# Performance work log

Measured on AMD Instinct MI355X. Metric: run time of the kernel, lower is better.

The kernel has to match this reference:

```python
import jax, jax.numpy as jnp
import numpy as np

EMBED_DIM = 512
HEADS = 8
ATTN_DIM = EMBED_DIM // HEADS
PF_DIM = 2048
B, L = 4, 2048
LN_EPS = 1e-5


def _linear(x, W, b):
    # nn.Linear: x @ W.T + b, W is [out, in]
    return jnp.einsum('bld,od->blo', x, W) + b


def _layer_norm(x, g, b):
    mu = jnp.mean(x, axis=-1, keepdims=True)
    var = jnp.mean(jnp.square(x - mu), axis=-1, keepdims=True)
    return (x - mu) * jax.lax.rsqrt(var + LN_EPS) * g + b


def _qkv(src, Wq, bq, Wk, bk, Wv, bv):
    def split(t):
        Bb, Ll, _ = t.shape
        return t.reshape(Bb, Ll, HEADS, ATTN_DIM).transpose(0, 2, 1, 3)  # [B,H,L,Dh]
    return (split(_linear(src, Wq, bq)),
            split(_linear(src, Wk, bk)),
            split(_linear(src, Wv, bv)))


def _attention(inp, Q, K1, K2, V1, V2, Wo, bo, ln_g, ln_b, W1, b1, W2, b2):
    # non-softmax linear attention: (Q K1^T) V1 + (Q K2^T) V2
    attn = (jnp.einsum('bhqk,bhkd->bhqd', jnp.einsum('bhqd,bhkd->bhqk', Q, K1), V1)
            + jnp.einsum('bhqk,bhkd->bhqd', jnp.einsum('bhqd,bhkd->bhqk', Q, K2), V2))
    Bb = Q.shape[0]
    attn = attn.transpose(0, 2, 1, 3).reshape(Bb, -1, HEADS * ATTN_DIM)  # [B,L,D]
    x = _linear(attn, Wo, bo)
    x = _layer_norm(inp + x, ln_g, ln_b)          # dropout p=0 (eval)
    ff = _linear(jax.nn.relu(_linear(x, W1, b1)), W2, b2)
    x = _layer_norm(x + ff, ln_g, ln_b)
    return x


def setup_inputs() -> dict:
    key = jax.random.key(0)
    ks = jax.random.split(key, 16)
    s = 0.02
    return {
        'question': jax.random.normal(ks[0], (B, L, EMBED_DIM), jnp.float32),
        'query': jax.random.normal(ks[1], (B, L, EMBED_DIM), jnp.float32),
        'Wq': jax.random.normal(ks[2], (EMBED_DIM, EMBED_DIM), jnp.float32) * s,
        'bq': jnp.zeros((EMBED_DIM,), jnp.float32),
        'Wk': jax.random.normal(ks[3], (EMBED_DIM, EMBED_DIM), jnp.float32) * s,
        'bk': jnp.zeros((EMBED_DIM,), jnp.float32),
        'Wv': jax.random.normal(ks[4], (EMBED_DIM, EMBED_DIM), jnp.float32) * s,
        'bv': jnp.zeros((EMBED_DIM,), jnp.float32),
        'Wo': jax.random.normal(ks[5], (EMBED_DIM, EMBED_DIM), jnp.float32) * s,
        'bo': jnp.zeros((EMBED_DIM,), jnp.float32),
        'ln_g': jnp.ones((EMBED_DIM,), jnp.float32),
        'ln_b': jnp.zeros((EMBED_DIM,), jnp.float32),
        'W1': jax.random.normal(ks[6], (PF_DIM, EMBED_DIM), jnp.float32) * s,
        'b1': jnp.zeros((PF_DIM,), jnp.float32),
        'W2': jax.random.normal(ks[7], (EMBED_DIM, PF_DIM), jnp.float32) * s,
        'b2': jnp.zeros((EMBED_DIM,), jnp.float32),
    }


def reference(question, query, Wq, bq, Wk, bk, Wv, bv, Wo, bo, ln_g, ln_b, W1, b1, W2, b2):
    Q1, K1, V1 = _qkv(question, Wq, bq, Wk, bk, Wv, bv)
    Q2, K2, V2 = _qkv(query, Wq, bq, Wk, bk, Wv, bv)
    question_attn = _attention(question, Q1, K1, K2, V1, V2, Wo, bo, ln_g, ln_b, W1, b1, W2, b2)
    query_attn = _attention(query, Q2, K2, K1, V2, V1, Wo, bo, ln_g, ln_b, W1, b1, W2, b2)
    return jnp.concatenate([question_attn, query_attn], axis=-1)
```

## Files before the change

kernel.cpp:

```cpp
#include <hip/hip_runtime.h>
#include <stdint.h>


#define Bq 4
#define Lq 2048
#define Dq 512
#define PFq 2048
#define Mrows 16384
#define MiBu 1048576ull
#define NSLICE 16

typedef __attribute__((ext_vector_type(8))) short frag_ab;
typedef __attribute__((ext_vector_type(4))) float frag_cd;
typedef __attribute__((ext_vector_type(8))) unsigned short ushort8v;

__device__ __forceinline__ unsigned short f2b(float f) {
    union { float f; uint32_t u; } x; x.f = f;
    uint32_t r = x.u + 0x7fffu + ((x.u >> 16) & 1u);
    return (unsigned short)(r >> 16);
}
__device__ __forceinline__ float b2f(unsigned short u) {
    union { uint32_t u; float f; } x; x.u = ((uint32_t)u) << 16;
    return x.f;
}

#define GLD16(g, l)                                                              \
    __builtin_amdgcn_global_load_lds(                                            \
        (const __attribute__((address_space(1))) void*)(const void*)(g),         \
        (__attribute__((address_space(3))) void*)(void*)(l), 16, 0, 0)

#define STG(BUFOFS, REGOFS, GB, ROWOFS, TILE, KS)                                \
    { GLD16((GB) + (size_t)(ROWOFS) * (KS) + (size_t)(TILE) * 64,                \
            Sh + (BUFOFS) + (REGOFS) + ld);                                      \
      GLD16((GB) + ((size_t)(ROWOFS) + 64) * (KS) + (size_t)(TILE) * 64,         \
            Sh + (BUFOFS) + (REGOFS) + ld + 4096); }

#define VMW(N) asm volatile("s_waitcnt vmcnt(" #N ")" ::: "memory")

#define PHASE(CB, M0, LOADB, STAGE_STMT, WAIT_STMT)                              \
    {                                                                            \
        frag_ab a00 = *(const frag_ab*)&Sh[(CB) + (wm + (M0)*16 + lr) * 64 + xo0];      \
        frag_ab a01 = *(const frag_ab*)&Sh[(CB) + (wm + (M0)*16 + lr) * 64 + xo1];      \
        frag_ab a10 = *(const frag_ab*)&Sh[(CB) + (wm + (M0)*16 + 16 + lr) * 64 + xo0]; \
        frag_ab a11 = *(const frag_ab*)&Sh[(CB) + (wm + (M0)*16 + 16 + lr) * 64 + xo1]; \
        if (LOADB) {                                                             \
            _Pragma("unroll")                                                    \
            for (int j = 0; j < 4; ++j) {                                        \
                bf[j][0] = *(const frag_ab*)&Sh[(CB) + 16384 + (wn + j*16 + lr)*64 + xo0]; \
                bf[j][1] = *(const frag_ab*)&Sh[(CB) + 16384 + (wn + j*16 + lr)*64 + xo1]; \
            }                                                                    \
        }                                                                        \
        STAGE_STMT;                                                              \
        WAIT_STMT;                                                               \
        __builtin_amdgcn_sched_barrier(0);                                       \
        __builtin_amdgcn_s_barrier();                                            \
        asm volatile("s_waitcnt lgkmcnt(0)" ::: "memory");                       \
        __builtin_amdgcn_sched_barrier(0);                                       \
        __builtin_amdgcn_s_setprio(1);                                           \
        _Pragma("unroll")                                                        \
        for (int j = 0; j < 4; ++j) {                                            \
            acc[(M0)][j]   = __builtin_amdgcn_mfma_f32_16x16x32_bf16(a00, bf[j][0], acc[(M0)][j], 0,0,0);   \
            acc[(M0)][j]   = __builtin_amdgcn_mfma_f32_16x16x32_bf16(a01, bf[j][1], acc[(M0)][j], 0,0,0);   \
            acc[(M0)+1][j] = __builtin_amdgcn_mfma_f32_16x16x32_bf16(a10, bf[j][0], acc[(M0)+1][j], 0,0,0); \
            acc[(M0)+1][j] = __builtin_amdgcn_mfma_f32_16x16x32_bf16(a11, bf[j][1], acc[(M0)+1][j], 0,0,0); \
        }                                                                        \
        __builtin_amdgcn_s_setprio(0);                                           \
        __builtin_amdgcn_sched_barrier(0);                                       \
        __builtin_amdgcn_s_barrier();                                            \
        __builtin_amdgcn_sched_barrier(0);                                       \
    }

__global__ __launch_bounds__(512, 2) void gemm_256(
    const unsigned short* __restrict__ A, const unsigned short* __restrict__ Wt,
    const float* __restrict__ bias, unsigned short* __restrict__ outB,
    int M, int N, int relu)
{
    __shared__ __align__(16) unsigned short Sh[65536];
    const int tid = threadIdx.x;
    const int lane = tid & 63;
    const int w = tid >> 6;
    const int wm = (w >> 2) * 128;
    const int wn = (w & 3) * 64;
    const int lr = lane & 15;
    const int quad = lane >> 4;
    const int xo0 = ((quad ^ (lr & 7)) << 3);
    const int xo1 = (((4 | quad) ^ (lr & 7)) << 3);

    const int b0 = blockIdx.x;
    const int xcd = b0 & 7, slot = b0 >> 3;
    const int mloc = (M >> 8) >> 3;
    const size_t bm = (size_t)(xcd * mloc + slot % mloc) * 256;
    const size_t bn = (size_t)(slot / mloc) * 256;

    const int ar = tid >> 3;
    const int sw = ((tid & 7) ^ (ar & 7)) << 3;
    const unsigned short* Ag = A  + (bm + ar) * (size_t)512 + sw;
    const unsigned short* Bg = Wt + (bn + ar) * (size_t)512 + sw;
    const int ld = tid * 8;

    frag_cd acc[8][4] = {};
    frag_ab bf[4][2];

    STG(0,     16384, Bg, 0,   0, 512);
    STG(0,     24576, Bg, 128, 0, 512);
    STG(0,     0,     Ag, 0,   0, 512);
    STG(0,     8192,  Ag, 128, 0, 512);
    STG(32768, 16384, Bg, 0,   1, 512);
    STG(32768, 24576, Bg, 128, 1, 512);
    VMW(4);
    __builtin_amdgcn_sched_barrier(0);
    __builtin_amdgcn_s_barrier();
    __builtin_amdgcn_sched_barrier(0);

    for (int I = 0; I < 3; ++I) {
        const int tb = 2 * I + 1, tc = 2 * I + 2, td = 2 * I + 3;
        PHASE(0,     0, 1, STG(32768, 0,     Ag, 0,   tb, 512), (void)0);
        PHASE(0,     2, 0, STG(32768, 8192,  Ag, 128, tb, 512), (void)0);
        PHASE(0,     4, 0, STG(0,     16384, Bg, 0,   tc, 512), (void)0);
        PHASE(0,     6, 0, STG(0,     24576, Bg, 128, tc, 512), VMW(4));
        PHASE(32768, 0, 1, STG(0,     0,     Ag, 0,   tc, 512), (void)0);
        PHASE(32768, 2, 0, STG(0,     8192,  Ag, 128, tc, 512), (void)0);
        PHASE(32768, 4, 0, STG(32768, 16384, Bg, 0,   td, 512), (void)0);
        PHASE(32768, 6, 0, STG(32768, 24576, Bg, 128, td, 512), VMW(4));
    }
    PHASE(0,     0, 1, STG(32768, 0,    Ag, 0,   7, 512), (void)0);
    PHASE(0,     2, 0, STG(32768, 8192, Ag, 128, 7, 512), (void)0);
    PHASE(0,     4, 0, (void)0, (void)0);
    PHASE(0,     6, 0, (void)0, VMW(0));
    PHASE(32768, 0, 1, (void)0, (void)0);
    PHASE(32768, 2, 0, (void)0, (void)0);
    PHASE(32768, 4, 0, (void)0, (void)0);
    PHASE(32768, 6, 0, (void)0, (void)0);

    float bv[4];
#pragma unroll
    for (int j = 0; j < 4; ++j) bv[j] = bias[(int)bn + wn + j * 16 + lr];
    unsigned short* Cs = Sh + w * 8192;
#pragma unroll
    for (int m = 0; m < 8; ++m)
#pragma unroll
        for (int j = 0; j < 4; ++j)
#pragma unroll
            for (int r = 0; r < 4; ++r) {
                float v = acc[m][j][r] + bv[j];
                if (relu) v = fmaxf(v, 0.f);
                Cs[(m * 16 + quad * 4 + r) * 64 + j * 16 + lr] = f2b(v);
            }
    const int rl = lane >> 3, c8 = (lane & 7) * 8;
#pragma unroll
    for (int k = 0; k < 16; ++k) {
        const int row = rl + k * 8;
        ushort8v val = *(const ushort8v*)&Cs[row * 64 + c8];
        *(ushort8v*)(outB + (size_t)(bm + wm + row) * N + bn + wn + c8) = val;
    }
}

__global__ __launch_bounds__(512, 2) void gemm_n128(
    const unsigned short* __restrict__ A, const unsigned short* __restrict__ Wt,
    const float* __restrict__ bias,
    const float* __restrict__ resA, const float* __restrict__ resB,
    const unsigned short* __restrict__ res16,
    unsigned short* __restrict__ outB, int N, int K, int mode, int perb)
{
    __shared__ __align__(16) unsigned short Sh[49152];
    const int tid = threadIdx.x;
    const int lane = tid & 63;
    const int w = tid >> 6;
    const int wm = (w >> 1) * 64;
    const int wn = (w & 1) * 64;
    const int lr = lane & 15;
    const int quad = lane >> 4;
    const int xo0 = ((quad ^ (lr & 7)) << 3);
    const int xo1 = (((4 | quad) ^ (lr & 7)) << 3);

    const int b0 = blockIdx.x;
    const int xcd = b0 & 7, slot = b0 >> 3;
    const size_t bm = (size_t)(xcd * 8 + (slot & 7)) * 256;
    const size_t bn = (size_t)(slot >> 3) * 128;

    if (perb) {
        const int bsel = ((int)(bm >> 11)) & 3;
        Wt += (size_t)bsel << 18;
        bias += bsel << 9;
    }

    const int ar = tid >> 3;
    const int sw = ((tid & 7) ^ (ar & 7)) << 3;
    const unsigned short* Ag = A  + (bm + ar) * (size_t)K + sw;
    const unsigned short* Bg = Wt + (bn + ar) * (size_t)K + sw;
    const int ld = tid * 8;

    frag_cd acc[4][4] = {};
    frag_ab bf[4][2];

    STG(0,     16384, Bg, 0,   0, K);
    STG(0,     0,     Ag, 0,   0, K);
    STG(0,     8192,  Ag, 128, 0, K);
    STG(24576, 16384, Bg, 0,   1, K);
    VMW(2);
    __builtin_amdgcn_sched_barrier(0);
    __builtin_amdgcn_s_barrier();
    __builtin_amdgcn_sched_barrier(0);

    const int nIter = K >> 7;
    for (int I = 0; I < nIter - 1; ++I) {
        const int tb = 2 * I + 1, tc = 2 * I + 2, td = 2 * I + 3;
        PHASE(0,     0, 1, { STG(24576, 0, Ag, 0, tb, K); STG(24576, 8192, Ag, 128, tb, K); }, (void)0);
        PHASE(0,     2, 0, STG(0, 16384, Bg, 0, tc, K), VMW(2));
        PHASE(24576, 0, 1, { STG(0, 0, Ag, 0, tc, K); STG(0, 8192, Ag, 128, tc, K); }, (void)0);
        PHASE(24576, 2, 0, STG(24576, 16384, Bg, 0, td, K), VMW(2));
    }
    {
        const int tb = (K >> 6) - 1;
        PHASE(0,     0, 1, { STG(24576, 0, Ag, 0, tb, K); STG(24576, 8192, Ag, 128, tb, K); }, (void)0);
        PHASE(0,     2, 0, (void)0, VMW(0));
        PHASE(24576, 0, 1, (void)0, (void)0);
        PHASE(24576, 2, 0, (void)0, (void)0);
    }

    float bv[4];
#pragma unroll
    for (int j = 0; j < 4; ++j) bv[j] = bias[(int)bn + wn + j * 16 + lr];
    unsigned short* Cs = Sh + w * 4096;
#pragma unroll
    for (int m = 0; m < 4; ++m)
#pragma unroll
        for (int j = 0; j < 4; ++j)
#pragma unroll
            for (int r = 0; r < 4; ++r)
                Cs[(m * 16 + quad * 4 + r) * 64 + j * 16 + lr] = f2b(acc[m][j][r] + bv[j]);
    const int rl = lane >> 3, c8 = (lane & 7) * 8;
#pragma unroll
    for (int k = 0; k < 8; ++k) {
        const int row = rl + k * 8;
        const int grow = (int)bm + wm + row;
        const size_t idx = (size_t)grow * N + bn + wn + c8;
        ushort8v val = *(const ushort8v*)&Cs[row * 64 + c8];
        if (mode == 0) {
            *(ushort8v*)(outB + idx) = val;
            continue;
        }
        float vv[8];
#pragma unroll
        for (int t2 = 0; t2 < 8; ++t2) vv[t2] = b2f(val[t2]);
        if (mode == 1) {
            const float* rp = (grow < 8192) ? resA + idx : resB + idx - (size_t)8192 * N;
            float4 ra = *(const float4*)(rp);
            float4 rb = *(const float4*)(rp + 4);
            vv[0] += ra.x; vv[1] += ra.y; vv[2] += ra.z; vv[3] += ra.w;
            vv[4] += rb.x; vv[5] += rb.y; vv[6] += rb.z; vv[7] += rb.w;
        } else {
            const unsigned short* rp16 = (mode == 2) ? (outB + idx) : (res16 + idx);
            ushort8v old = *(const ushort8v*)rp16;
#pragma unroll
            for (int t2 = 0; t2 < 8; ++t2) vv[t2] += b2f(old[t2]);
        }
        ushort8v o;
#pragma unroll
        for (int t2 = 0; t2 < 8; ++t2) o[t2] = f2b(vv[t2]);
        *(ushort8v*)(outB + idx) = o;
    }
}

__global__ __launch_bounds__(256) void gemm_fuse(
    const unsigned short* __restrict__ Wob, const unsigned short* __restrict__ UT,
    unsigned short* __restrict__ Wfin)
{
    __shared__ __align__(16) unsigned short Sh[2 * 128 * 64];
    unsigned short* At = Sh;
    unsigned short* Bt = Sh + 128 * 64;
    const int tid = threadIdx.x;
    const int lane = tid & 63;
    const int w = tid >> 6;
    const int wm = (w >> 1) * 64, wn = (w & 1) * 64;
    const int lr = lane & 15;
    const int quad = lane >> 4;
    const int bb = blockIdx.z;
    const size_t bm = (size_t)blockIdx.x * 128, bn = (size_t)blockIdx.y * 128;

    frag_cd acc[4][4] = {};
    const int ar = tid >> 3;
    const int acs = (((tid & 7) ^ (ar & 7)) << 3);
    const unsigned short* Ag = Wob + (bm + ar) * 512 + acs;
    const unsigned short* Bg = UT + ((size_t)bb << 18) + (bn + ar) * 512 + acs;
    unsigned short* Asd = At + w * 512;
    unsigned short* Bsd = Bt + w * 512;

    for (int k0 = 0; k0 < 512; k0 += 64) {
        __syncthreads();
#pragma unroll
        for (int i = 0; i < 4; ++i) {
            GLD16(Ag + (size_t)(32 * i) * 512 + k0, Asd + i * 2048);
            GLD16(Bg + (size_t)(32 * i) * 512 + k0, Bsd + i * 2048);
        }
        __syncthreads();
#pragma unroll
        for (int kk = 0; kk < 2; ++kk) {
            frag_ab a[4], b[4];
#pragma unroll
            for (int i = 0; i < 4; ++i)
                a[i] = *(const frag_ab*)&At[(wm + i * 16 + lr) * 64 +
                                            ((((kk << 2) | quad) ^ (lr & 7)) << 3)];
#pragma unroll
            for (int j = 0; j < 4; ++j)
                b[j] = *(const frag_ab*)&Bt[(wn + j * 16 + lr) * 64 +
                                            ((((kk << 2) | quad) ^ (lr & 7)) << 3)];
#pragma unroll
            for (int i = 0; i < 4; ++i)
#pragma unroll
                for (int j = 0; j < 4; ++j)
                    acc[i][j] = __builtin_amdgcn_mfma_f32_16x16x32_bf16(a[i], b[j], acc[i][j], 0, 0, 0);
        }
    }
    __syncthreads();
    unsigned short* Cs = Sh + w * 4096;
#pragma unroll
    for (int j = 0; j < 4; ++j)
#pragma unroll
        for (int i = 0; i < 4; ++i)
#pragma unroll
            for (int r = 0; r < 4; ++r)
                Cs[(i * 16 + quad * 4 + r) * 64 + j * 16 + lr] = f2b(acc[i][j][r]);
    const int rl = lane >> 3, c8 = (lane & 7) * 8;
#pragma unroll
    for (int k = 0; k < 8; ++k) {
        const int row = rl + k * 8;
        ushort8v val = *(const ushort8v*)&Cs[row * 64 + c8];
        *(ushort8v*)(Wfin + ((size_t)bb << 18) + (bm + wm + row) * 512 + bn + wn + c8) = val;
    }
}

__global__ __launch_bounds__(256) void convert_all(
    const float* __restrict__ Wq, const float* __restrict__ Wk,
    const float* __restrict__ Wv, const float* __restrict__ Wo,
    const float* __restrict__ W1, const float* __restrict__ W2,
    const float* __restrict__ question, const float* __restrict__ query,
    const float* __restrict__ bqp, const float* __restrict__ bkp,
    const float* __restrict__ bvp, const float* __restrict__ bo,
    unsigned short* __restrict__ Wqkvb, unsigned short* __restrict__ Wob,
    unsigned short* __restrict__ W1b, unsigned short* __restrict__ W2b,
    unsigned short* __restrict__ Xb, float* __restrict__ bqkv,
    float* __restrict__ biasO)
{
    const int b = blockIdx.x;
    const float* src; unsigned short* dst; size_t off;
    if (b < 256)        { src = Wq; dst = Wqkvb;          off = (size_t)b * 1024; }
    else if (b < 512)   { src = Wk; dst = Wqkvb + 262144; off = (size_t)(b - 256) * 1024; }
    else if (b < 768)   { src = Wv; dst = Wqkvb + 524288; off = (size_t)(b - 512) * 1024; }
    else if (b < 1024)  { src = Wo; dst = Wob;            off = (size_t)(b - 768) * 1024; }
    else if (b < 2048)  { src = W1; dst = W1b;            off = (size_t)(b - 1024) * 1024; }
    else if (b < 3072)  { src = W2; dst = W2b;            off = (size_t)(b - 2048) * 1024; }
    else if (b < 7168)  { src = question; dst = Xb;       off = (size_t)(b - 3072) * 1024; }
    else if (b < 11264) { src = query; dst = Xb + 4194304; off = (size_t)(b - 7168) * 1024; }
    else if (b < 11270) {
        const int n = (b - 11264) * 256 + threadIdx.x;
        bqkv[n] = (n < 512) ? bqp[n] : (n < 1024) ? bkp[n - 512] : bvp[n - 1024];
        return;
    } else {
        const int n = (b - 11270) * 256 + threadIdx.x;
        biasO[n] = bo[n & 511];
        return;
    }
    const size_t idx = off + threadIdx.x * 4;
    float4 v = *(const float4*)(src + idx);
    ushort4 o;
    o.x = f2b(v.x); o.y = f2b(v.y); o.z = f2b(v.z); o.w = f2b(v.w);
    *(ushort4*)(dst + idx) = o;
}

__global__ __launch_bounds__(256) void s_kernel(
    const unsigned short* __restrict__ QKV, float* __restrict__ Spart)
{
    const int bh = blockIdx.x;
    const int sl = blockIdx.y;
    const int b = bh >> 3, h = bh & 7;
    const int pass = sl >> 3;
    const int l0 = (sl & 7) * 256;
    __shared__ float Ks[64][64];
    __shared__ float Vs[64][64];
    const int tid = threadIdx.x;
    const int tx = tid & 15, ty = tid >> 4;
    const int srow = tid >> 3;
    const int scol = (tid & 7) * 8;
    const size_t rowbase = (size_t)pass * 8192 + (size_t)b * Lq + l0;

    float acc[4][4] = {};

    for (int t0 = 0; t0 < 256; t0 += 64) {
        const unsigned short* kp0 = QKV + (rowbase + t0 + srow) * 1024 + h * 64 + scol;
        const unsigned short* kp1 = kp0 + (size_t)32 * 1024;
        ushort8v k0 = *(const ushort8v*)kp0;
        ushort8v v0 = *(const ushort8v*)(kp0 + 512);
        ushort8v k1 = *(const ushort8v*)kp1;
        ushort8v v1 = *(const ushort8v*)(kp1 + 512);
        __syncthreads();
#pragma unroll
        for (int e = 0; e < 8; ++e) {
            Ks[srow][scol + e]      = b2f(k0[e]);
            Vs[srow][scol + e]      = b2f(v0[e]);
            Ks[srow + 32][scol + e] = b2f(k1[e]);
            Vs[srow + 32][scol + e] = b2f(v1[e]);
        }
        __syncthreads();
#pragma unroll 4
        for (int rr = 0; rr < 64; ++rr) {
            const float4 kf = *(const float4*)&Ks[rr][ty * 4];
            const float4 vf = *(const float4*)&Vs[rr][tx * 4];
            acc[0][0] = fmaf(kf.x, vf.x, acc[0][0]);
            acc[0][1] = fmaf(kf.x, vf.y, acc[0][1]);
            acc[0][2] = fmaf(kf.x, vf.z, acc[0][2]);
            acc[0][3] = fmaf(kf.x, vf.w, acc[0][3]);
            acc[1][0] = fmaf(kf.y, vf.x, acc[1][0]);
            acc[1][1] = fmaf(kf.y, vf.y, acc[1][1]);
            acc[1][2] = fmaf(kf.y, vf.z, acc[1][2]);
            acc[1][3] = fmaf(kf.y, vf.w, acc[1][3]);
            acc[2][0] = fmaf(kf.z, vf.x, acc[2][0]);
            acc[2][1] = fmaf(kf.z, vf.y, acc[2][1]);
            acc[2][2] = fmaf(kf.z, vf.z, acc[2][2]);
            acc[2][3] = fmaf(kf.z, vf.w, acc[2][3]);
            acc[3][0] = fmaf(kf.w, vf.x, acc[3][0]);
            acc[3][1] = fmaf(kf.w, vf.y, acc[3][1]);
            acc[3][2] = fmaf(kf.w, vf.z, acc[3][2]);
            acc[3][3] = fmaf(kf.w, vf.w, acc[3][3]);
        }
    }

    float* Sp = Spart + ((size_t)bh * NSLICE + sl) * 4096;
#pragma unroll
    for (int i = 0; i < 4; ++i) {
        float4 o = make_float4(acc[i][0], acc[i][1], acc[i][2], acc[i][3]);
        *(float4*)(Sp + (ty * 4 + i) * 64 + tx * 4) = o;
    }
}

__global__ __launch_bounds__(512) void u_kernel(
    const float* __restrict__ Spart, const unsigned short* __restrict__ Wqb,
    const unsigned short* __restrict__ Wob, const float* __restrict__ bq,
    unsigned short* __restrict__ UT, float* __restrict__ biasO)
{
    const int bh = blockIdx.x, jh = blockIdx.y;
    const int b = bh >> 3, h = bh & 7;
    __shared__ float Sf[4096];
    __shared__ float rsh[32];
    const int t = threadIdx.x;
    const float* Sp = Spart + (size_t)bh * (NSLICE * 4096);
#pragma unroll
    for (int e = 0; e < 8; ++e) {
        const int d = e * 512 + t;
        float v = 0.f;
#pragma unroll
        for (int s = 0; s < NSLICE; ++s) v += Sp[(size_t)s * 4096 + d];
        Sf[d] = v;
    }
    __syncthreads();

    const int j0 = jh * 32;
    float T[32] = {};
    for (int k = 0; k < 64; ++k) {
        const float wq = b2f(Wqb[(h * 64 + k) * 512 + t]);
#pragma unroll
        for (int j = 0; j < 32; ++j)
            T[j] = fmaf(wq, Sf[k * 64 + j0 + j], T[j]);
    }
    unsigned short* up = UT + ((size_t)(b * 512 + t)) * 512 + h * 64 + j0;
#pragma unroll
    for (int g = 0; g < 4; ++g) {
        ushort8v o;
#pragma unroll
        for (int e = 0; e < 8; ++e) o[e] = f2b(T[g * 8 + e]);
        *(ushort8v*)(up + g * 8) = o;
    }

    if (t < 32) {
        float r = 0.f;
        for (int k = 0; k < 64; ++k) r += bq[h * 64 + k] * Sf[k * 64 + j0 + t];
        rsh[t] = r;
    }
    __syncthreads();
    float c = 0.f;
#pragma unroll
    for (int j = 0; j < 32; ++j)
        c += rsh[j] * b2f(Wob[(size_t)t * 512 + h * 64 + j0 + j]);
    atomicAdd(&biasO[b * 512 + t], c);
}

__global__ __launch_bounds__(256) void ln_b16_inplace(
    unsigned short* __restrict__ Y, const float* __restrict__ g,
    const float* __restrict__ bta)
{
    __shared__ float part[8];
    const int row = blockIdx.x;
    const int t = threadIdx.x;
    const int w = t >> 6;
    unsigned short* yr = Y + (size_t)row * Dq;
    const float v0 = b2f(yr[t]), v1 = b2f(yr[t + 256]);
    float s = v0 + v1;
#pragma unroll
    for (int off = 32; off; off >>= 1) s += __shfl_xor(s, off, 64);
    if ((t & 63) == 0) part[w] = s;
    __syncthreads();
    const float mean = (part[0] + part[1] + part[2] + part[3]) * (1.f / Dq);
    const float d0 = v0 - mean, d1 = v1 - mean;
    float q = d0 * d0 + d1 * d1;
#pragma unroll
    for (int off = 32; off; off >>= 1) q += __shfl_xor(q, off, 64);
    if ((t & 63) == 0) part[4 + w] = q;
    __syncthreads();
    const float rstd = rsqrtf((part[4] + part[5] + part[6] + part[7]) * (1.f / Dq) + 1e-5f);
    yr[t] = f2b(d0 * rstd * g[t] + bta[t]);
    yr[t + 256] = f2b(d1 * rstd * g[t + 256] + bta[t + 256]);
}

__global__ __launch_bounds__(256) void ln_b16_out(
    const unsigned short* __restrict__ Y, const float* __restrict__ g,
    const float* __restrict__ bta, float* __restrict__ out)
{
    __shared__ float part[8];
    const int row = blockIdx.x;
    const int t = threadIdx.x;
    const int w = t >> 6;
    const unsigned short* yr = Y + (size_t)row * Dq;
    const float v0 = b2f(yr[t]), v1 = b2f(yr[t + 256]);
    float s = v0 + v1;
#pragma unroll
    for (int off = 32; off; off >>= 1) s += __shfl_xor(s, off, 64);
    if ((t & 63) == 0) part[w] = s;
    __syncthreads();
    const float mean = (part[0] + part[1] + part[2] + part[3]) * (1.f / Dq);
    const float d0 = v0 - mean, d1 = v1 - mean;
    float q = d0 * d0 + d1 * d1;
#pragma unroll
    for (int off = 32; off; off >>= 1) q += __shfl_xor(q, off, 64);
    if ((t & 63) == 0) part[4 + w] = q;
    __syncthreads();
    const float rstd = rsqrtf((part[4] + part[5] + part[6] + part[7]) * (1.f / Dq) + 1e-5f);
    const int half = row >> 13, br = row & 8191;
    float* orow = out + (size_t)br * 1024 + half * 512;
    orow[t] = d0 * rstd * g[t] + bta[t];
    orow[t + 256] = d1 * rstd * g[t + 256] + bta[t + 256];
}

extern "C" void kernel_launch(void* const* d_in, const int* in_sizes, int n_in,
                              void* d_out, int out_size, void* d_ws, size_t ws_size,
                              hipStream_t stream)
{
    const float* question = (const float*)d_in[0];
    const float* query    = (const float*)d_in[1];
    const float* Wq = (const float*)d_in[2];  const float* bqp = (const float*)d_in[3];
    const float* Wk = (const float*)d_in[4];  const float* bkp = (const float*)d_in[5];
    const float* Wv = (const float*)d_in[6];  const float* bvp = (const float*)d_in[7];
    const float* Wo = (const float*)d_in[8];  const float* bo  = (const float*)d_in[9];
    const float* ln_g = (const float*)d_in[10]; const float* ln_b = (const float*)d_in[11];
    const float* W1 = (const float*)d_in[12]; const float* b1 = (const float*)d_in[13];
    const float* W2 = (const float*)d_in[14]; const float* b2 = (const float*)d_in[15];
    float* out = (float*)d_out;
    char* ws = (char*)d_ws;

    unsigned short* QKVb = (unsigned short*)(ws);
    unsigned short* UT   = (unsigned short*)(ws + 32 * MiBu);
    unsigned short* Wfin = (unsigned short*)(ws + 34 * MiBu);
    float* Spart         = (float*)(ws + 40 * MiBu);
    unsigned short* hb   = (unsigned short*)(ws);
    unsigned short* xbuf = (unsigned short*)(ws + 64 * MiBu);
    unsigned short* Xb   = (unsigned short*)d_out;
    char* wp = ws + 80 * MiBu;
    unsigned short* Wqkvb = (unsigned short*)wp;  wp += 1536 * 512 * 2;
    unsigned short* Wob   = (unsigned short*)wp;  wp += 512 * 512 * 2;
    unsigned short* W1b   = (unsigned short*)wp;  wp += 2048 * 512 * 2;
    unsigned short* W2b   = (unsigned short*)wp;  wp += 512 * 2048 * 2;
    float* biasO          = (float*)wp;           wp += 4 * 512 * 4;
    float* bqkv           = (float*)wp;

    dim3 blk(256);

    convert_all<<<11278, blk, 0, stream>>>(Wq, Wk, Wv, Wo, W1, W2, question, query,
                                           bqp, bkp, bvp, bo,
                                           Wqkvb, Wob, W1b, W2b, Xb, bqkv, biasO);

    gemm_256<<<dim3(256), dim3(512), 0, stream>>>(Xb, Wqkvb + 262144, bqkv + 512,
                                                  QKVb, Mrows, 1024, 0);

    s_kernel<<<dim3(32, NSLICE), blk, 0, stream>>>(QKVb, Spart);
    u_kernel<<<dim3(32, 2), dim3(512), 0, stream>>>(Spart, Wqkvb, Wob, bqkv, UT, biasO);
    gemm_fuse<<<dim3(4, 4, 4), blk, 0, stream>>>(Wob, UT, Wfin);

    gemm_n128<<<dim3(256), dim3(512), 0, stream>>>(Xb, Wfin, biasO,
                                                   nullptr, nullptr, Xb, xbuf,
                                                   512, 512, 3, 1);

    ln_b16_inplace<<<Mrows, blk, 0, stream>>>(xbuf, ln_g, ln_b);

    gemm_256<<<dim3(512), dim3(512), 0, stream>>>(xbuf, W1b, b1, hb,
                                                  Mrows, PFq, 1);

    gemm_n128<<<dim3(256), dim3(512), 0, stream>>>(hb, W2b, b2,
                                                   nullptr, nullptr, nullptr, xbuf,
                                                   512, 2048, 2, 0);

    ln_b16_out<<<Mrows, blk, 0, stream>>>(xbuf, ln_g, ln_b, out);
}
```

Measured before the change: 310.2 us.

## Merge all stages into one cooperative persistent kernel with grid syncs

New measurement: 638.2 us. 2.06x slower.

```diff
diff --git a/kernel.cpp b/kernel.cpp
--- a/kernel.cpp
+++ b/kernel.cpp
@@ -1,8 +1,10 @@
 #include <hip/hip_runtime.h>
+#include <hip/hip_cooperative_groups.h>
 #include <stdint.h>
 
-
-#define Bq 4
+namespace cg = cooperative_groups;
+
+
 #define Lq 2048
 #define Dq 512
 #define PFq 2048
@@ -70,12 +72,11 @@
         __builtin_amdgcn_sched_barrier(0);                                       \
     }
 
-__global__ __launch_bounds__(512, 2) void gemm_256(
+__device__ __forceinline__ void dev_gemm256(
     const unsigned short* __restrict__ A, const unsigned short* __restrict__ Wt,
     const float* __restrict__ bias, unsigned short* __restrict__ outB,
-    int M, int N, int relu)
-{
-    __shared__ __align__(16) unsigned short Sh[65536];
+    int M, int N, int relu, int b0, unsigned short* Sh)
+{
     const int tid = threadIdx.x;
     const int lane = tid & 63;
     const int w = tid >> 6;
@@ -86,7 +87,6 @@
     const int xo0 = ((quad ^ (lr & 7)) << 3);
     const int xo1 = (((4 | quad) ^ (lr & 7)) << 3);
 
-    const int b0 = blockIdx.x;
     const int xcd = b0 & 7, slot = b0 >> 3;
     const int mloc = (M >> 8) >> 3;
     const size_t bm = (size_t)(xcd * mloc + slot % mloc) * 256;
@@ -155,14 +155,12 @@
     }
 }
 
-__global__ __launch_bounds__(512, 2) void gemm_n128(
+__device__ __forceinline__ void dev_gemmn128(
     const unsigned short* __restrict__ A, const unsigned short* __restrict__ Wt,
-    const float* __restrict__ bias,
-    const float* __restrict__ resA, const float* __restrict__ resB,
-    const unsigned short* __restrict__ res16,
-    unsigned short* __restrict__ outB, int N, int K, int mode, int perb)
-{
-    __shared__ __align__(16) unsigned short Sh[49152];
+    const float* __restrict__ bias, const unsigned short* __restrict__ res16,
+    unsigned short* __restrict__ outB, int N, int K, int mode, int perb,
+    int b0, unsigned short* Sh)
+{
     const int tid = threadIdx.x;
     const int lane = tid & 63;
     const int w = tid >> 6;
@@ -173,7 +171,6 @@
     const int xo0 = ((quad ^ (lr & 7)) << 3);
     const int xo1 = (((4 | quad) ^ (lr & 7)) << 3);
 
-    const int b0 = blockIdx.x;
     const int xcd = b0 & 7, slot = b0 >> 3;
     const size_t bm = (size_t)(xcd * 8 + (slot & 7)) * 256;
     const size_t bn = (size_t)(slot >> 3) * 128;
@@ -243,13 +240,7 @@
         float vv[8];
 #pragma unroll
         for (int t2 = 0; t2 < 8; ++t2) vv[t2] = b2f(val[t2]);
-        if (mode == 1) {
-            const float* rp = (grow < 8192) ? resA + idx : resB + idx - (size_t)8192 * N;
-            float4 ra = *(const float4*)(rp);
-            float4 rb = *(const float4*)(rp + 4);
-            vv[0] += ra.x; vv[1] += ra.y; vv[2] += ra.z; vv[3] += ra.w;
-            vv[4] += rb.x; vv[5] += rb.y; vv[6] += rb.z; vv[7] += rb.w;
-        } else {
+        {
             const unsigned short* rp16 = (mode == 2) ? (outB + idx) : (res16 + idx);
             ushort8v old = *(const ushort8v*)rp16;
 #pragma unroll
@@ -262,126 +253,18 @@
     }
 }
 
-__global__ __launch_bounds__(256) void gemm_fuse(
-    const unsigned short* __restrict__ Wob, const unsigned short* __restrict__ UT,
-    unsigned short* __restrict__ Wfin)
-{
-    __shared__ __align__(16) unsigned short Sh[2 * 128 * 64];
-    unsigned short* At = Sh;
-    unsigned short* Bt = Sh + 128 * 64;
-    const int tid = threadIdx.x;
-    const int lane = tid & 63;
-    const int w = tid >> 6;
-    const int wm = (w >> 1) * 64, wn = (w & 1) * 64;
-    const int lr = lane & 15;
-    const int quad = lane >> 4;
-    const int bb = blockIdx.z;
-    const size_t bm = (size_t)blockIdx.x * 128, bn = (size_t)blockIdx.y * 128;
-
-    frag_cd acc[4][4] = {};
-    const int ar = tid >> 3;
-    const int acs = (((tid & 7) ^ (ar & 7)) << 3);
-    const unsigned short* Ag = Wob + (bm + ar) * 512 + acs;
-    const unsigned short* Bg = UT + ((size_t)bb << 18) + (bn + ar) * 512 + acs;
-    unsigned short* Asd = At + w * 512;
-    unsigned short* Bsd = Bt + w * 512;
-
-    for (int k0 = 0; k0 < 512; k0 += 64) {
-        __syncthreads();
-#pragma unroll
-        for (int i = 0; i < 4; ++i) {
-            GLD16(Ag + (size_t)(32 * i) * 512 + k0, Asd + i * 2048);
-            GLD16(Bg + (size_t)(32 * i) * 512 + k0, Bsd + i * 2048);
-        }
-        __syncthreads();
-#pragma unroll
-        for (int kk = 0; kk < 2; ++kk) {
-            frag_ab a[4], b[4];
-#pragma unroll
-            for (int i = 0; i < 4; ++i)
-                a[i] = *(const frag_ab*)&At[(wm + i * 16 + lr) * 64 +
-                                            ((((kk << 2) | quad) ^ (lr & 7)) << 3)];
-#pragma unroll
-            for (int j = 0; j < 4; ++j)
-                b[j] = *(const frag_ab*)&Bt[(wn + j * 16 + lr) * 64 +
-                                            ((((kk << 2) | quad) ^ (lr & 7)) << 3)];
-#pragma unroll
-            for (int i = 0; i < 4; ++i)
-#pragma unroll
-                for (int j = 0; j < 4; ++j)
-                    acc[i][j] = __builtin_amdgcn_mfma_f32_16x16x32_bf16(a[i], b[j], acc[i][j], 0, 0, 0);
-        }
-    }
-    __syncthreads();
-    unsigned short* Cs = Sh + w * 4096;
-#pragma unroll
-    for (int j = 0; j < 4; ++j)
-#pragma unroll
-        for (int i = 0; i < 4; ++i)
-#pragma unroll
-            for (int r = 0; r < 4; ++r)
-                Cs[(i * 16 + quad * 4 + r) * 64 + j * 16 + lr] = f2b(acc[i][j][r]);
-    const int rl = lane >> 3, c8 = (lane & 7) * 8;
-#pragma unroll
-    for (int k = 0; k < 8; ++k) {
-        const int row = rl + k * 8;
-        ushort8v val = *(const ushort8v*)&Cs[row * 64 + c8];
-        *(ushort8v*)(Wfin + ((size_t)bb << 18) + (bm + wm + row) * 512 + bn + wn + c8) = val;
-    }
-}
-
-__global__ __launch_bounds__(256) void convert_all(
-    const float* __restrict__ Wq, const float* __restrict__ Wk,
-    const float* __restrict__ Wv, const float* __restrict__ Wo,
-    const float* __restrict__ W1, const float* __restrict__ W2,
-    const float* __restrict__ question, const float* __restrict__ query,
-    const float* __restrict__ bqp, const float* __restrict__ bkp,
-    const float* __restrict__ bvp, const float* __restrict__ bo,
-    unsigned short* __restrict__ Wqkvb, unsigned short* __restrict__ Wob,
-    unsigned short* __restrict__ W1b, unsigned short* __restrict__ W2b,
-    unsigned short* __restrict__ Xb, float* __restrict__ bqkv,
-    float* __restrict__ biasO)
-{
-    const int b = blockIdx.x;
-    const float* src; unsigned short* dst; size_t off;
-    if (b < 256)        { src = Wq; dst = Wqkvb;          off = (size_t)b * 1024; }
-    else if (b < 512)   { src = Wk; dst = Wqkvb + 262144; off = (size_t)(b - 256) * 1024; }
-    else if (b < 768)   { src = Wv; dst = Wqkvb + 524288; off = (size_t)(b - 512) * 1024; }
-    else if (b < 1024)  { src = Wo; dst = Wob;            off = (size_t)(b - 768) * 1024; }
-    else if (b < 2048)  { src = W1; dst = W1b;            off = (size_t)(b - 1024) * 1024; }
-    else if (b < 3072)  { src = W2; dst = W2b;            off = (size_t)(b - 2048) * 1024; }
-    else if (b < 7168)  { src = question; dst = Xb;       off = (size_t)(b - 3072) * 1024; }
-    else if (b < 11264) { src = query; dst = Xb + 4194304; off = (size_t)(b - 7168) * 1024; }
-    else if (b < 11270) {
-        const int n = (b - 11264) * 256 + threadIdx.x;
-        bqkv[n] = (n < 512) ? bqp[n] : (n < 1024) ? bkp[n - 512] : bvp[n - 1024];
-        return;
-    } else {
-        const int n = (b - 11270) * 256 + threadIdx.x;
-        biasO[n] = bo[n & 511];
-        return;
-    }
-    const size_t idx = off + threadIdx.x * 4;
-    float4 v = *(const float4*)(src + idx);
-    ushort4 o;
-    o.x = f2b(v.x); o.y = f2b(v.y); o.z = f2b(v.z); o.w = f2b(v.w);
-    *(ushort4*)(dst + idx) = o;
-}
-
-__global__ __launch_bounds__(256) void s_kernel(
-    const unsigned short* __restrict__ QKV, float* __restrict__ Spart)
-{
-    const int bh = blockIdx.x;
-    const int sl = blockIdx.y;
+__device__ __forceinline__ void dev_s(
+    const unsigned short* __restrict__ QKV, float* __restrict__ Spart,
+    int vb, int t, float* Ks, float* Vs)
+{
+    const int bh = vb >> 4;
+    const int sl = vb & 15;
     const int b = bh >> 3, h = bh & 7;
     const int pass = sl >> 3;
     const int l0 = (sl & 7) * 256;
-    __shared__ float Ks[64][64];
-    __shared__ float Vs[64][64];
-    const int tid = threadIdx.x;
-    const int tx = tid & 15, ty = tid >> 4;
-    const int srow = tid >> 3;
-    const int scol = (tid & 7) * 8;
+    const int tx = t & 15, ty = t >> 4;
+    const int srow = t >> 3;
+    const int scol = (t & 7) * 8;
     const size_t rowbase = (size_t)pass * 8192 + (size_t)b * Lq + l0;
 
     float acc[4][4] = {};
@@ -396,16 +279,16 @@
         __syncthreads();
 #pragma unroll
         for (int e = 0; e < 8; ++e) {
-            Ks[srow][scol + e]      = b2f(k0[e]);
-            Vs[srow][scol + e]      = b2f(v0[e]);
-            Ks[srow + 32][scol + e] = b2f(k1[e]);
-            Vs[srow + 32][scol + e] = b2f(v1[e]);
+            Ks[srow * 64 + scol + e]        = b2f(k0[e]);
+            Vs[srow * 64 + scol + e]        = b2f(v0[e]);
+            Ks[(srow + 32) * 64 + scol + e] = b2f(k1[e]);
+            Vs[(srow + 32) * 64 + scol + e] = b2f(v1[e]);
         }
         __syncthreads();
 #pragma unroll 4
         for (int rr = 0; rr < 64; ++rr) {
-            const float4 kf = *(const float4*)&Ks[rr][ty * 4];
-            const float4 vf = *(const float4*)&Vs[rr][tx * 4];
+            const float4 kf = *(const float4*)&Ks[rr * 64 + ty * 4];
+            const float4 vf = *(const float4*)&Vs[rr * 64 + tx * 4];
             acc[0][0] = fmaf(kf.x, vf.x, acc[0][0]);
             acc[0][1] = fmaf(kf.x, vf.y, acc[0][1]);
             acc[0][2] = fmaf(kf.x, vf.z, acc[0][2]);
@@ -433,15 +316,13 @@
     }
 }
 
-__global__ __launch_bounds__(512) void u_kernel(
+__device__ __forceinline__ void dev_u(
     const float* __restrict__ Spart, const unsigned short* __restrict__ Wqb,
     const unsigned short* __restrict__ Wob, const float* __restrict__ bq,
-    unsigned short* __restrict__ UT, float* __restrict__ biasO)
-{
-    const int bh = blockIdx.x, jh = blockIdx.y;
+    unsigned short* __restrict__ UT, float* __restrict__ biasO,
+    int bh, int jh, float* Sf, float* rsh)
+{
     const int b = bh >> 3, h = bh & 7;
-    __shared__ float Sf[4096];
-    __shared__ float rsh[32];
     const int t = threadIdx.x;
     const float* Sp = Spart + (size_t)bh * (NSLICE * 4096);
 #pragma unroll
@@ -484,60 +365,210 @@
     atomicAdd(&biasO[b * 512 + t], c);
 }
 
-__global__ __launch_bounds__(256) void ln_b16_inplace(
+__device__ __forceinline__ void dev_fuse(
+    const unsigned short* __restrict__ Wob, const unsigned short* __restrict__ UT,
+    unsigned short* __restrict__ Wfin, int vb, int t, unsigned short* Sh)
+{
+    unsigned short* At = Sh;
+    unsigned short* Bt = Sh + 128 * 64;
+    const int lane = t & 63;
+    const int w = t >> 6;
+    const int wm = (w >> 1) * 64, wn = (w & 1) * 64;
+    const int lr = lane & 15;
+    const int quad = lane >> 4;
+    const int bb = vb >> 4;
+    const size_t bm = (size_t)(vb & 3) * 128, bn = (size_t)((vb >> 2) & 3) * 128;
+
+    frag_cd acc[4][4] = {};
+    const int ar = t >> 3;
+    const int acs = (((t & 7) ^ (ar & 7)) << 3);
+    const unsigned short* Ag = Wob + (bm + ar) * 512 + acs;
+    const unsigned short* Bg = UT + ((size_t)bb << 18) + (bn + ar) * 512 + acs;
+    unsigned short* Asd = At + w * 512;
+    unsigned short* Bsd = Bt + w * 512;
+
+    for (int k0 = 0; k0 < 512; k0 += 64) {
+        __syncthreads();
+#pragma unroll
+        for (int i = 0; i < 4; ++i) {
+            GLD16(Ag + (size_t)(32 * i) * 512 + k0, Asd + i * 2048);
+            GLD16(Bg + (size_t)(32 * i) * 512 + k0, Bsd + i * 2048);
+        }
+        __syncthreads();
+#pragma unroll
+        for (int kk = 0; kk < 2; ++kk) {
+            frag_ab a[4], b[4];
+#pragma unroll
+            for (int i = 0; i < 4; ++i)
+                a[i] = *(const frag_ab*)&At[(wm + i * 16 + lr) * 64 +
+                                            ((((kk << 2) | quad) ^ (lr & 7)) << 3)];
+#pragma unroll
+            for (int j = 0; j < 4; ++j)
+                b[j] = *(const frag_ab*)&Bt[(wn + j * 16 + lr) * 64 +
+                                            ((((kk << 2) | quad) ^ (lr & 7)) << 3)];
+#pragma unroll
+            for (int i = 0; i < 4; ++i)
+#pragma unroll
+                for (int j = 0; j < 4; ++j)
+                    acc[i][j] = __builtin_amdgcn_mfma_f32_16x16x32_bf16(a[i], b[j], acc[i][j], 0, 0, 0);
+        }
+    }
+    __syncthreads();
+    unsigned short* Cs = Sh + w * 4096;
+#pragma unroll
+    for (int j = 0; j < 4; ++j)
+#pragma unroll
+        for (int i = 0; i < 4; ++i)
+#pragma unroll
+            for (int r = 0; r < 4; ++r)
+                Cs[(i * 16 + quad * 4 + r) * 64 + j * 16 + lr] = f2b(acc[i][j][r]);
+    const int rl = lane >> 3, c8 = (lane & 7) * 8;
+#pragma unroll
+    for (int k = 0; k < 8; ++k) {
+        const int row = rl + k * 8;
+        ushort8v val = *(const ushort8v*)&Cs[row * 64 + c8];
+        *(ushort8v*)(Wfin + ((size_t)bb << 18) + (bm + wm + row) * 512 + bn + wn + c8) = val;
+    }
+}
+
+__device__ __forceinline__ void dev_ln(
     unsigned short* __restrict__ Y, const float* __restrict__ g,
-    const float* __restrict__ bta)
-{
-    __shared__ float part[8];
-    const int row = blockIdx.x;
-    const int t = threadIdx.x;
-    const int w = t >> 6;
-    unsigned short* yr = Y + (size_t)row * Dq;
-    const float v0 = b2f(yr[t]), v1 = b2f(yr[t + 256]);
-    float s = v0 + v1;
-#pragma unroll
-    for (int off = 32; off; off >>= 1) s += __shfl_xor(s, off, 64);
-    if ((t & 63) == 0) part[w] = s;
+    const float* __restrict__ bta, float* __restrict__ out, int blk, int tid)
+{
+    const int wv = tid >> 6, lane = tid & 63;
+    const int c0 = lane * 8;
+    float4 ga = *(const float4*)(g + c0), gb = *(const float4*)(g + c0 + 4);
+    float4 ba = *(const float4*)(bta + c0), bb = *(const float4*)(bta + c0 + 4);
+    const float gv[8] = {ga.x, ga.y, ga.z, ga.w, gb.x, gb.y, gb.z, gb.w};
+    const float bv[8] = {ba.x, ba.y, ba.z, ba.w, bb.x, bb.y, bb.z, bb.w};
+#pragma unroll
+    for (int r = 0; r < 8; ++r) {
+        const int row = blk * 64 + r * 8 + wv;
+        unsigned short* yr = Y + (size_t)row * Dq;
+        ushort8v v = *(const ushort8v*)(yr + c0);
+        float f[8];
+        float s = 0.f;
+#pragma unroll
+        for (int e = 0; e < 8; ++e) { f[e] = b2f(v[e]); s += f[e]; }
+#pragma unroll
+        for (int off = 32; off; off >>= 1) s += __shfl_xor(s, off, 64);
+        const float mean = s * (1.f / Dq);
+        float q = 0.f;
+#pragma unroll
+        for (int e = 0; e < 8; ++e) { f[e] -= mean; q += f[e] * f[e]; }
+#pragma unroll
+        for (int off = 32; off; off >>= 1) q += __shfl_xor(q, off, 64);
+        const float rstd = rsqrtf(q * (1.f / Dq) + 1e-5f);
+        if (out) {
+            const int half = row >> 13, br = row & 8191;
+            float* orow = out + (size_t)br * 1024 + half * 512 + c0;
+            float4 o0, o1;
+            o0.x = f[0] * rstd * gv[0] + bv[0];
+            o0.y = f[1] * rstd * gv[1] + bv[1];
+            o0.z = f[2] * rstd * gv[2] + bv[2];
+            o0.w = f[3] * rstd * gv[3] + bv[3];
+            o1.x = f[4] * rstd * gv[4] + bv[4];
+            o1.y = f[5] * rstd * gv[5] + bv[5];
+            o1.z = f[6] * rstd * gv[6] + bv[6];
+            o1.w = f[7] * rstd * gv[7] + bv[7];
+            *(float4*)orow = o0;
+            *(float4*)(orow + 4) = o1;
+        } else {
+            ushort8v o;
+#pragma unroll
+            for (int e = 0; e < 8; ++e) o[e] = f2b(f[e] * rstd * gv[e] + bv[e]);
+            *(ushort8v*)(yr + c0) = o;
+        }
+    }
+}
+
+__global__ __launch_bounds__(512, 2) void mega(
+    const float* __restrict__ question, const float* __restrict__ query,
+    const float* __restrict__ Wq, const float* __restrict__ bqp,
+    const float* __restrict__ Wk, const float* __restrict__ bkp,
+    const float* __restrict__ Wv, const float* __restrict__ bvp,
+    const float* __restrict__ Wo, const float* __restrict__ bo,
+    const float* __restrict__ ln_g, const float* __restrict__ ln_b,
+    const float* __restrict__ W1, const float* __restrict__ b1,
+    const float* __restrict__ W2, const float* __restrict__ b2,
+    float* __restrict__ out,
+    unsigned short* __restrict__ QKVb, unsigned short* __restrict__ UT,
+    unsigned short* __restrict__ Wfin, float* __restrict__ Spart,
+    unsigned short* __restrict__ Xb, unsigned short* __restrict__ xbuf,
+    unsigned short* __restrict__ hb,
+    unsigned short* __restrict__ Wqkvb, unsigned short* __restrict__ Wob,
+    unsigned short* __restrict__ W1b, unsigned short* __restrict__ W2b,
+    float* __restrict__ biasO, float* __restrict__ bqkv)
+{
+    __shared__ __align__(16) unsigned short Sh[65536];
+    cg::grid_group grid = cg::this_grid();
+    const int blk = blockIdx.x;
+    const int tid = threadIdx.x;
+
+    for (int vb = blk * 2 + (tid >> 8); vb < 11278; vb += 512) {
+        const int t = tid & 255;
+        const float* src; unsigned short* dst; size_t off;
+        if (vb < 256)        { src = Wq; dst = Wqkvb;          off = (size_t)vb * 1024; }
+        else if (vb < 512)   { src = Wk; dst = Wqkvb + 262144; off = (size_t)(vb - 256) * 1024; }
+        else if (vb < 768)   { src = Wv; dst = Wqkvb + 524288; off = (size_t)(vb - 512) * 1024; }
+        else if (vb < 1024)  { src = Wo; dst = Wob;            off = (size_t)(vb - 768) * 1024; }
+        else if (vb < 2048)  { src = W1; dst = W1b;            off = (size_t)(vb - 1024) * 1024; }
+        else if (vb < 3072)  { src = W2; dst = W2b;            off = (size_t)(vb - 2048) * 1024; }
+        else if (vb < 7168)  { src = question; dst = Xb;       off = (size_t)(vb - 3072) * 1024; }
+        else if (vb < 11264) { src = query; dst = Xb + 4194304; off = (size_t)(vb - 7168) * 1024; }
+        else if (vb < 11270) {
+            const int n = (vb - 11264) * 256 + t;
+            bqkv[n] = (n < 512) ? bqp[n] : (n < 1024) ? bkp[n - 512] : bvp[n - 1024];
+            continue;
+        } else {
+            const int n = (vb - 11270) * 256 + t;
+            biasO[n] = bo[n & 511];
+            continue;
+        }
+        const size_t idx = off + t * 4;
+        float4 v = *(const float4*)(src + idx);
+        ushort4 o;
+        o.x = f2b(v.x); o.y = f2b(v.y); o.z = f2b(v.z); o.w = f2b(v.w);
+        *(ushort4*)(dst + idx) = o;
+    }
+    grid.sync();
+
+    dev_gemm256(Xb, Wqkvb + 262144, bqkv + 512, QKVb, Mrows, 1024, 0, blk, Sh);
+    grid.sync();
+
+    {
+        const int sub = tid >> 8, t = tid & 255;
+        float* base = (float*)Sh + sub * 8192;
+        dev_s(QKVb, Spart, blk * 2 + sub, t, base, base + 4096);
+    }
+    grid.sync();
+
+    if (blk < 64)
+        dev_u(Spart, Wqkvb, Wob, bqkv, UT, biasO, blk >> 1, blk & 1,
+              (float*)Sh, (float*)Sh + 4096);
+    grid.sync();
+
+    if (blk < 32) {
+        const int sub = tid >> 8, t = tid & 255;
+        dev_fuse(Wob, UT, Wfin, blk * 2 + sub, t, Sh + sub * 16384);
+    }
+    grid.sync();
+
+    dev_gemmn128(Xb, Wfin, biasO, Xb, xbuf, 512, 512, 3, 1, blk, Sh);
+    grid.sync();
+
+    dev_ln(xbuf, ln_g, ln_b, nullptr, blk, tid);
+    grid.sync();
+
+    dev_gemm256(xbuf, W1b, b1, hb, Mrows, PFq, 1, blk, Sh);
     __syncthreads();
-    const float mean = (part[0] + part[1] + part[2] + part[3]) * (1.f / Dq);
-    const float d0 = v0 - mean, d1 = v1 - mean;
-    float q = d0 * d0 + d1 * d1;
-#pragma unroll
-    for (int off = 32; off; off >>= 1) q += __shfl_xor(q, off, 64);
-    if ((t & 63) == 0) part[4 + w] = q;
-    __syncthreads();
-    const float rstd = rsqrtf((part[4] + part[5] + part[6] + part[7]) * (1.f / Dq) + 1e-5f);
-    yr[t] = f2b(d0 * rstd * g[t] + bta[t]);
-    yr[t + 256] = f2b(d1 * rstd * g[t + 256] + bta[t + 256]);
-}
-
-__global__ __launch_bounds__(256) void ln_b16_out(
-    const unsigned short* __restrict__ Y, const float* __restrict__ g,
-    const float* __restrict__ bta, float* __restrict__ out)
-{
-    __shared__ float part[8];
-    const int row = blockIdx.x;
-    const int t = threadIdx.x;
-    const int w = t >> 6;
-    const unsigned short* yr = Y + (size_t)row * Dq;
-    const float v0 = b2f(yr[t]), v1 = b2f(yr[t + 256]);
-    float s = v0 + v1;
-#pragma unroll
-    for (int off = 32; off; off >>= 1) s += __shfl_xor(s, off, 64);
-    if ((t & 63) == 0) part[w] = s;
-    __syncthreads();
-    const float mean = (part[0] + part[1] + part[2] + part[3]) * (1.f / Dq);
-    const float d0 = v0 - mean, d1 = v1 - mean;
-    float q = d0 * d0 + d1 * d1;
-#pragma unroll
-    for (int off = 32; off; off >>= 1) q += __shfl_xor(q, off, 64);
-    if ((t & 63) == 0) part[4 + w] = q;
-    __syncthreads();
-    const float rstd = rsqrtf((part[4] + part[5] + part[6] + part[7]) * (1.f / Dq) + 1e-5f);
-    const int half = row >> 13, br = row & 8191;
-    float* orow = out + (size_t)br * 1024 + half * 512;
-    orow[t] = d0 * rstd * g[t] + bta[t];
-    orow[t + 256] = d1 * rstd * g[t + 256] + bta[t + 256];
+    dev_gemm256(xbuf, W1b, b1, hb, Mrows, PFq, 1, blk + 256, Sh);
+    grid.sync();
+
+    dev_gemmn128(hb, W2b, b2, nullptr, xbuf, 512, 2048, 2, 0, blk, Sh);
+    grid.sync();
+
+    dev_ln(xbuf, ln_g, ln_b, out, blk, tid);
 }
 
 extern "C" void kernel_launch(void* const* d_in, const int* in_sizes, int n_in,
@@ -560,9 +591,9 @@
     unsigned short* UT   = (unsigned short*)(ws + 32 * MiBu);
     unsigned short* Wfin = (unsigned short*)(ws + 34 * MiBu);
     float* Spart         = (float*)(ws + 40 * MiBu);
+    unsigned short* Xb   = (unsigned short*)(ws + 48 * MiBu);
     unsigned short* hb   = (unsigned short*)(ws);
     unsigned short* xbuf = (unsigned short*)(ws + 64 * MiBu);
-    unsigned short* Xb   = (unsigned short*)d_out;
     char* wp = ws + 80 * MiBu;
     unsigned short* Wqkvb = (unsigned short*)wp;  wp += 1536 * 512 * 2;
     unsigned short* Wob   = (unsigned short*)wp;  wp += 512 * 512 * 2;
@@ -571,31 +602,17 @@
     float* biasO          = (float*)wp;           wp += 4 * 512 * 4;
     float* bqkv           = (float*)wp;
 
-    dim3 blk(256);
-
-    convert_all<<<11278, blk, 0, stream>>>(Wq, Wk, Wv, Wo, W1, W2, question, query,
-                                           bqp, bkp, bvp, bo,
-                                           Wqkvb, Wob, W1b, W2b, Xb, bqkv, biasO);
-
-    gemm_256<<<dim3(256), dim3(512), 0, stream>>>(Xb, Wqkvb + 262144, bqkv + 512,
-                                                  QKVb, Mrows, 1024, 0);
-
-    s_kernel<<<dim3(32, NSLICE), blk, 0, stream>>>(QKVb, Spart);
-    u_kernel<<<dim3(32, 2), dim3(512), 0, stream>>>(Spart, Wqkvb, Wob, bqkv, UT, biasO);
-    gemm_fuse<<<dim3(4, 4, 4), blk, 0, stream>>>(Wob, UT, Wfin);
-
-    gemm_n128<<<dim3(256), dim3(512), 0, stream>>>(Xb, Wfin, biasO,
-                                                   nullptr, nullptr, Xb, xbuf,
-                                                   512, 512, 3, 1);
-
-    ln_b16_inplace<<<Mrows, blk, 0, stream>>>(xbuf, ln_g, ln_b);
-
-    gemm_256<<<dim3(512), dim3(512), 0, stream>>>(xbuf, W1b, b1, hb,
-                                                  Mrows, PFq, 1);
-
-    gemm_n128<<<dim3(256), dim3(512), 0, stream>>>(hb, W2b, b2,
-                                                   nullptr, nullptr, nullptr, xbuf,
-                                                   512, 2048, 2, 0);
-
-    ln_b16_out<<<Mrows, blk, 0, stream>>>(xbuf, ln_g, ln_b, out);
-}
+    void* args[] = {
+        (void*)&question, (void*)&query,
+        (void*)&Wq, (void*)&bqp, (void*)&Wk, (void*)&bkp, (void*)&Wv, (void*)&bvp,
+        (void*)&Wo, (void*)&bo, (void*)&ln_g, (void*)&ln_b,
+        (void*)&W1, (void*)&b1, (void*)&W2, (void*)&b2,
+        (void*)&out,
+        (void*)&QKVb, (void*)&UT, (void*)&Wfin, (void*)&Spart,
+        (void*)&Xb, (void*)&xbuf, (void*)&hb,
+        (void*)&Wqkvb, (void*)&Wob, (void*)&W1b, (void*)&W2b,
+        (void*)&biasO, (void*)&bqkv
+    };
+    hipLaunchCooperativeKernel((const void*)mega, dim3(256), dim3(512),
+                               args, 0, stream);
+}
```
